# Optimization experiments

Hardware: AMD Instinct MI355X
Metric: run time of the kernel (lower is better)

Reference implementation:

```python
import jax, jax.numpy as jnp
import numpy as np

N_NODES = 49
FEAT_DIM = 1280            # efficientnet_v2_s feature dim
NODE_DIM = FEAT_DIM // N_NODES  # 26
GAT_HID = 256
HEADS = 4
NUM_CLASSES = 5
BATCH = 8192


def _grid_edges():
    # 7x7 grid, 8-neighborhood, as in _create_grid_edges, plus PyG default self loops
    edges = []
    for i in range(7):
        for j in range(7):
            node = i * 7 + j
            for di in (-1, 0, 1):
                for dj in (-1, 0, 1):
                    if di == 0 and dj == 0:
                        continue
                    ni, nj = i + di, j + dj
                    if 0 <= ni < 7 and 0 <= nj < 7:
                        edges.append((node, ni * 7 + nj))
    edges += [(n, n) for n in range(N_NODES)]  # add_self_loops=True (PyG default)
    return np.asarray(edges, dtype=np.int64).T  # [2, 361]


def setup_inputs() -> dict:
    key = jax.random.key(0)
    ks = jax.random.split(key, 16)
    s = 0.05
    inp = {
        "x": jax.random.normal(ks[0], (BATCH, FEAT_DIM), jnp.float32),
        "transform_w": jax.random.normal(ks[1], (FEAT_DIM, N_NODES * NODE_DIM), jnp.float32) * s,
        "transform_b": jnp.zeros((N_NODES * NODE_DIM,), jnp.float32),
        # GATv2 layer 1: 26 -> 64 per head, 4 heads, concat -> 256
        "g1_wl": jax.random.normal(ks[2], (NODE_DIM, GAT_HID), jnp.float32) * s,
        "g1_wr": jax.random.normal(ks[3], (NODE_DIM, GAT_HID), jnp.float32) * s,
        "g1_att": jax.random.normal(ks[4], (HEADS, GAT_HID // HEADS), jnp.float32) * s,
        "g1_b": jnp.zeros((GAT_HID,), jnp.float32),
        # GATv2 layer 2: 256 -> 256, 1 head, mean
        "g2_wl": jax.random.normal(ks[5], (GAT_HID, GAT_HID), jnp.float32) * s,
        "g2_wr": jax.random.normal(ks[6], (GAT_HID, GAT_HID), jnp.float32) * s,
        "g2_att": jax.random.normal(ks[7], (1, GAT_HID), jnp.float32) * s,
        "g2_b": jnp.zeros((GAT_HID,), jnp.float32),
        "fc_w": jax.random.normal(ks[8], (NODE_DIM + GAT_HID, NUM_CLASSES), jnp.float32) * s,
        "fc_b": jnp.zeros((NUM_CLASSES,), jnp.float32),
        "edge_index": jnp.asarray(_grid_edges()),
    }
    return inp


def _gatv2(x, src, dst, wl, wr, att, b, heads, out_ch, concat):
    # PyG GATv2Conv (share_weights=False, negative_slope=0.2, eval mode)
    n = x.shape[0]
    xl = (x @ wl).reshape(n, heads, out_ch)  # source messages
    xr = (x @ wr).reshape(n, heads, out_ch)  # target side of attention
    e = jax.nn.leaky_relu(xl[src] + xr[dst], 0.2)        # [E, H, C]
    score = jnp.einsum('ehc,hc->eh', e, att)             # [E, H]
    smax = jax.ops.segment_max(score, dst, num_segments=n)
    ex = jnp.exp(score - smax[dst])
    den = jax.ops.segment_sum(ex, dst, num_segments=n)
    alpha = ex / den[dst]                                # softmax over in-edges per node
    out = jax.ops.segment_sum(xl[src] * alpha[..., None], dst, num_segments=n)  # [N,H,C]
    out = out.reshape(n, heads * out_ch) if concat else out.mean(axis=1)
    return out + b


def reference(x, transform_w, transform_b, g1_wl, g1_wr, g1_att, g1_b,
              g2_wl, g2_wr, g2_att, g2_b, fc_w, fc_b, edge_index):
    src, dst = edge_index[0], edge_index[1]
    node = (x @ transform_w + transform_b).reshape(-1, N_NODES, NODE_DIM)  # [B,49,26]

    def graph(nf):
        h = _gatv2(nf, src, dst, g1_wl, g1_wr, g1_att, g1_b, HEADS, GAT_HID // HEADS, True)
        h = jax.nn.elu(h)  # dropout inactive in eval
        h = _gatv2(h, src, dst, g2_wl, g2_wr, g2_att, g2_b, 1, GAT_HID, False)
        return h  # [49, 256]

    g = jax.vmap(graph)(node)                              # [B,49,256]
    pooled = jnp.concatenate([node, g], axis=-1).mean(axis=1)  # [B, 282]
    return pooled @ fc_w + fc_b
```

## Files before the change

### kernel.cpp

```cpp
#include <hip/hip_runtime.h>
#include <hip/hip_bf16.h>

typedef __bf16 bf16;
typedef __attribute__((ext_vector_type(8))) __bf16 bf16x8;
typedef __attribute__((ext_vector_type(4))) float f32x4;

constexpr int BATCH = 8192, NN = 49, ND = 26, NOUT = 1274, FD = 1280;
constexpr int HID = 256, NE = 361, HEADS = 4;
constexpr int KT_X = 40;
constexpr int MT_X = 512;
constexpr int NB_W = 10;
constexpr int NTB  = 9;

constexpr size_t OFF_XPACK = 0;
constexpr size_t SZ_XPACK  = (size_t)MT_X * KT_X * 512 * 2;
constexpr size_t OFF_WPACK = OFF_XPACK + SZ_XPACK;
constexpr size_t SZ_WPACK  = (size_t)NB_W * NTB * KT_X * 512 * 2;
constexpr size_t OFF_B1    = OFF_WPACK + SZ_WPACK;
constexpr size_t SZ_B1     = (size_t)32 * 512 * 2;
constexpr size_t OFF_B2    = OFF_B1 + SZ_B1;
constexpr size_t SZ_B2     = (size_t)32 * 8 * 512 * 2;
constexpr size_t OFF_N32   = OFF_B2 + SZ_B2;
constexpr size_t SZ_N32    = (size_t)BATCH * NN * 32 * 2;
constexpr size_t OFF_PN    = OFF_N32 + SZ_N32;
constexpr size_t SZ_PN     = (size_t)BATCH * ND * 4;
constexpr size_t OFF_CSR   = OFF_PN + SZ_PN;
constexpr size_t SZ_CSR    = 8192;
constexpr size_t OFF_CHUNK = OFF_CSR + SZ_CSR;


__global__ __launch_bounds__(256) void k_pack_x(const float* __restrict__ x,
                                                bf16* __restrict__ xp) {
    int g = blockIdx.x * 256 + threadIdx.x;
    int lane = g & 63, frag = g >> 6;
    int mt = frag / KT_X, kt = frag - mt * KT_X;
    int row = mt * 16 + (lane & 15);
    int k0  = kt * 32 + (lane >> 4) * 8;
    const float* src = x + (size_t)row * FD + k0;
    bf16x8 v;
#pragma unroll
    for (int j = 0; j < 8; ++j) v[j] = (bf16)src[j];
    *(bf16x8*)(xp + ((size_t)frag * 64 + lane) * 8) = v;
}

__global__ __launch_bounds__(256) void k_pack_w(const float* __restrict__ w,
                                                bf16* __restrict__ wp) {
    int g = blockIdx.x * 256 + threadIdx.x;
    int lane = g & 63, frag = g >> 6;
    int kt = frag % KT_X, t2 = frag / KT_X;
    int nt = t2 % NTB, nb = t2 / NTB;
    int col = nb * 130 + nt * 16 + (lane & 15);
    int k0  = kt * 32 + (lane >> 4) * 8;
    bool ok = (col < NOUT) && (col < nb * 130 + 130);
    bf16x8 v;
#pragma unroll
    for (int j = 0; j < 8; ++j)
        v[j] = ok ? (bf16)w[(size_t)(k0 + j) * NOUT + col] : (bf16)0.f;
    *(bf16x8*)(wp + ((size_t)frag * 64 + lane) * 8) = v;
}

__global__ __launch_bounds__(256) void k_pack_g1(const float* __restrict__ wl,
                                                 const float* __restrict__ wr,
                                                 bf16* __restrict__ bp) {
    int g = blockIdx.x * 256 + threadIdx.x;
    int lane = g & 63, nt = g >> 6;
    int n  = nt * 16 + (lane & 15);
    int k0 = (lane >> 4) * 8;
    bf16x8 v;
#pragma unroll
    for (int j = 0; j < 8; ++j) {
        int k = k0 + j;
        float f = 0.f;
        if (k < ND) f = (n < HID) ? wl[k * HID + n] : wr[k * HID + (n - HID)];
        v[j] = (bf16)f;
    }
    *(bf16x8*)(bp + ((size_t)nt * 64 + lane) * 8) = v;
}

__global__ __launch_bounds__(256) void k_pack_g2(const float* __restrict__ wl,
                                                 const float* __restrict__ wr,
                                                 bf16* __restrict__ bp) {
    int g = blockIdx.x * 256 + threadIdx.x;
    int lane = g & 63, frag = g >> 6;
    int nt = frag >> 3, kt = frag & 7;
    int n  = nt * 16 + (lane & 15);
    int k0 = kt * 32 + (lane >> 4) * 8;
    bf16x8 v;
#pragma unroll
    for (int j = 0; j < 8; ++j) {
        int k = k0 + j;
        float f = (n < HID) ? wl[k * HID + n] : wr[k * HID + (n - HID)];
        v[j] = (bf16)f;
    }
    *(bf16x8*)(bp + ((size_t)frag * 64 + lane) * 8) = v;
}

__global__ __launch_bounds__(128) void k_csr_par(const int* __restrict__ ei,
                                                 int* __restrict__ csr) {
    __shared__ int es[NE], ed[NE], cnt[NN], ocnt[NN], off[NN + 1], ooff[NN + 1];
    int tid = threadIdx.x;
    if (tid < NN) { cnt[tid] = 0; ocnt[tid] = 0; }
    for (int e = tid; e < NE; e += 128) { es[e] = ei[e]; ed[e] = ei[NE + e]; }
    __syncthreads();
    for (int e = tid; e < NE; e += 128) {
        atomicAdd(&cnt[ed[e]], 1);
        atomicAdd(&ocnt[es[e]], 1);
    }
    __syncthreads();
    if (tid == 0) {
        off[0] = 0; ooff[0] = 0;
        for (int n = 0; n < NN; ++n) {
            off[n + 1] = off[n] + cnt[n];
            ooff[n + 1] = ooff[n] + ocnt[n];
        }
    }
    __syncthreads();
    if (tid < NN) {
        int p = off[tid];
        for (int e = 0; e < NE; ++e)
            if (ed[e] == tid) { csr[50 + p] = e; csr[411 + p] = es[e]; ++p; }
    } else if (tid >= 64 && tid < 64 + NN) {
        int n = tid - 64;
        int p = ooff[n];
        for (int e = 0; e < NE; ++e)
            if (es[e] == n) { csr[822 + p] = e; ++p; }
    }
    if (tid < 50) { csr[tid] = off[tid]; csr[772 + tid] = ooff[tid]; }
}

__global__ __launch_bounds__(256, 2) void k_gemm_node(const bf16* __restrict__ xp,
                                                      const bf16* __restrict__ wp,
                                                      const float* __restrict__ tb,
                                                      bf16* __restrict__ node32) {
    __shared__ bf16 L[128][148];
    __shared__ float tbS[144];
    int tid = threadIdx.x, lane = tid & 63, w = tid >> 6;
    int nb = blockIdx.y, C0 = nb * 130;
    int mt0 = blockIdx.x * 16 + w * 4;
    if (tid < 144) { int col = C0 + tid; tbS[tid] = (col < NOUT) ? tb[col] : 0.f; }
    f32x4 acc[4][9] = {};
    const bf16* wpB = wp + (size_t)(nb * NTB) * KT_X * 512;
    for (int kt = 0; kt < KT_X; ++kt) {
        bf16x8 a[4];
#pragma unroll
        for (int i = 0; i < 4; ++i)
            a[i] = *(const bf16x8*)(xp + (((size_t)(mt0 + i) * KT_X + kt) * 64 + lane) * 8);
#pragma unroll
        for (int j = 0; j < NTB; ++j) {
            bf16x8 b = *(const bf16x8*)(wpB + ((size_t)(j * KT_X + kt) * 64 + lane) * 8);
#pragma unroll
            for (int i = 0; i < 4; ++i)
                acc[i][j] = __builtin_amdgcn_mfma_f32_16x16x32_bf16(a[i], b, acc[i][j], 0, 0, 0);
        }
    }
    int c0 = lane & 15, r0 = (lane >> 4) * 4;
    int nodes = (nb == 9) ? 4 : 5;
    int total = 128 * nodes * 4;
    for (int half = 0; half < 2; ++half) {
        __syncthreads();
        if ((w >> 1) == half) {
            int lrbase = (w & 1) * 64;
#pragma unroll
            for (int i = 0; i < 4; ++i) {
#pragma unroll
                for (int j = 0; j < NTB; ++j) {
                    int col = j * 16 + c0;
                    float bias = tbS[col];
#pragma unroll
                    for (int r = 0; r < 4; ++r)
                        L[lrbase + i * 16 + r0 + r][col] = (bf16)(acc[i][j][r] + bias);
                }
            }
        }
        __syncthreads();
        int B0 = blockIdx.x * 256 + half * 128;
        for (int t = tid; t < total; t += 256) {
            int q = t & 3, t2 = t >> 2;
            int n_l = t2 % nodes, brow = t2 / nodes;
            bf16x8 o;
#pragma unroll
            for (int jj = 0; jj < 8; ++jj) {
                int d = q * 8 + jj;
                o[jj] = (d < ND) ? L[brow][n_l * 26 + d] : (bf16)0.f;
            }
            *(bf16x8*)(node32 + (((size_t)(B0 + brow) * NN + nb * 5 + n_l) * 32 + q * 8)) = o;
        }
    }
}

__global__ __launch_bounds__(256) void k_pool(const bf16* __restrict__ node32,
                                              float* __restrict__ pN) {
    int b = blockIdx.x * 8 + (threadIdx.x >> 5);
    int d = threadIdx.x & 31;
    if (d >= ND) return;
    const bf16* base = node32 + (size_t)b * NN * 32 + d;
    float s = 0.f;
    for (int n = 0; n < NN; ++n) s += (float)base[n * 32];
    pN[b * ND + d] = s;
}

__global__ __launch_bounds__(512, 2) void k_fuse1(const bf16* __restrict__ n32,
                                                  const bf16* __restrict__ B1p,
                                                  bf16* __restrict__ h1f,
                                                  const float* __restrict__ att1,
                                                  const float* __restrict__ g1b,
                                                  const int* __restrict__ ei,
                                                  const int* __restrict__ csr) {
    __shared__ __align__(16) char X[NN * 1024];
    __shared__ __align__(16) float attS[256];
    __shared__ float sc[NE * 4], srden[NN * 4], bS[256];
    __shared__ int ieOff[50], ieId[NE], ieSrc[NE], srcS[NE], dstS[NE];

    int tid = threadIdx.x, lane = tid & 63, w = tid >> 6, g = blockIdx.x;

    for (int i = tid; i < 256; i += 512) { attS[i] = att1[i]; bS[i] = g1b[i]; }
    for (int i = tid; i < NE; i += 512) {
        srcS[i] = ei[i]; dstS[i] = ei[NE + i];
        ieId[i] = csr[50 + i]; ieSrc[i] = csr[411 + i];
    }
    if (tid < 50) ieOff[tid] = csr[tid];

    {
        int mt = w & 3, ng = w >> 2;
        int arow = mt * 16 + (lane & 15);
        bf16x8 a = {};
        if (arow < NN)
            a = *(const bf16x8*)(n32 + ((size_t)(g * NN + arow) * 32 + (lane >> 4) * 8));
        f32x4 acc[16];
#pragma unroll
        for (int j = 0; j < 16; ++j) {
            f32x4 z = {0.f, 0.f, 0.f, 0.f};
            bf16x8 b = *(const bf16x8*)(B1p + ((size_t)(ng * 16 + j) * 64 + lane) * 8);
            acc[j] = __builtin_amdgcn_mfma_f32_16x16x32_bf16(a, b, z, 0, 0, 0);
        }
        int c0 = lane & 15, r0 = (lane >> 4) * 4;
#pragma unroll
        for (int j = 0; j < 16; ++j) {
            int col = (ng * 16 + j) * 16 + c0;
#pragma unroll
            for (int r = 0; r < 4; ++r) {
                int n = mt * 16 + r0 + r;
                if (n < NN)
                    *(bf16*)(X + n * 1024 + ((col * 2) ^ ((n & 7) << 4))) = (bf16)acc[j][r];
            }
        }
    }
    __syncthreads();

    int rot = tid & 7;
    for (int task = tid; task < NE * 4; task += 512) {
        int h = task / NE, e = task - h * NE;
        int s = srcS[e], d = dstS[e];
        int sws = (s & 7) << 4, swd = (d & 7) << 4;
        const char* ps = X + s * 1024;
        const char* pd = X + d * 1024;
        float pa[4] = {0.f, 0.f, 0.f, 0.f};
#pragma unroll
        for (int i = 0; i < 8; ++i) {
            int cc = ((i + rot) & 7) * 8;
            bf16x8 xl = *(const bf16x8*)(ps + (((h * 64 + cc) * 2) ^ sws));
            bf16x8 xr = *(const bf16x8*)(pd + (((256 + h * 64 + cc) * 2) ^ swd));
            float4 a0 = *(const float4*)(attS + h * 64 + cc);
            float4 a1 = *(const float4*)(attS + h * 64 + cc + 4);
            const float aa[8] = {a0.x, a0.y, a0.z, a0.w, a1.x, a1.y, a1.z, a1.w};
#pragma unroll
            for (int q = 0; q < 8; ++q) {
                float v = (float)xl[q] + (float)xr[q];
                v = v > 0.f ? v : 0.2f * v;
                pa[q & 3] = fmaf(aa[q], v, pa[q & 3]);
            }
        }
        sc[e * 4 + h] = (pa[0] + pa[1]) + (pa[2] + pa[3]);
    }
    __syncthreads();
    for (int t = tid; t < NN * 4; t += 512) {
        int n = t >> 2, h = t & 3;
        float m = -1e30f;
        for (int j = ieOff[n]; j < ieOff[n + 1]; ++j) m = fmaxf(m, sc[ieId[j] * 4 + h]);
        float den = 0.f;
        for (int j = ieOff[n]; j < ieOff[n + 1]; ++j) {
            int idx = ieId[j] * 4 + h;
            float ex = __expf(sc[idx] - m);
            sc[idx] = ex; den += ex;
        }
        srden[t] = 1.f / den;
    }
    __syncthreads();
    for (int task = tid; task < NN * 32; task += 512) {
        int n = task >> 5, cb = task & 31;
        int ch0 = cb * 8, hh = cb >> 3;
        float a8[8] = {};
        int j0 = ieOff[n], j1 = ieOff[n + 1];
        for (int j = j0; j < j1; ++j) {
            float al = sc[ieId[j] * 4 + hh];
            int s = ieSrc[j];
            bf16x8 xv = *(const bf16x8*)(X + s * 1024 + ((ch0 * 2) ^ ((s & 7) << 4)));
#pragma unroll
            for (int q = 0; q < 8; ++q) a8[q] = fmaf(al, (float)xv[q], a8[q]);
        }
        float rs = srden[n * 4 + hh];
        bf16x8 o;
#pragma unroll
        for (int q = 0; q < 8; ++q) {
            float v = fmaf(a8[q], rs, bS[ch0 + q]);
            v = v > 0.f ? v : (__expf(v) - 1.f);
            o[q] = (bf16)v;
        }
        int Rl = g * NN + n;
        int kt = ch0 >> 5, kg = (ch0 >> 3) & 3;
        size_t addr = (((size_t)(Rl >> 4) * 8 + kt) * 64 + (Rl & 15) + 16 * kg) * 8;
        *(bf16x8*)(h1f + addr) = o;
    }
}

__global__ __launch_bounds__(256) void k_gemm_l2(const bf16* __restrict__ Af,
                                                 const bf16* __restrict__ Bf,
                                                 bf16* __restrict__ xlr) {
    __shared__ bf16 LT[128][136];
    int tid = threadIdx.x, lane = tid & 63, w = tid >> 6;
    int mtb = blockIdx.x * 8 + (w >> 1) * 4;
    int ntb = blockIdx.y * 8 + (w & 1) * 4;
    f32x4 acc[4][4] = {};
    for (int kt = 0; kt < 8; ++kt) {
        bf16x8 a[4], b[4];
#pragma unroll
        for (int i = 0; i < 4; ++i)
            a[i] = *(const bf16x8*)(Af + (((size_t)(mtb + i) * 8 + kt) * 64 + lane) * 8);
#pragma unroll
        for (int j = 0; j < 4; ++j)
            b[j] = *(const bf16x8*)(Bf + (((size_t)(ntb + j) * 8 + kt) * 64 + lane) * 8);
#pragma unroll
        for (int i = 0; i < 4; ++i)
#pragma unroll
            for (int j = 0; j < 4; ++j)
                acc[i][j] = __builtin_amdgcn_mfma_f32_16x16x32_bf16(a[i], b[j], acc[i][j], 0, 0, 0);
    }
    int c0 = lane & 15, r0 = (lane >> 4) * 4;
    int lr0 = (w >> 1) * 64, lc0 = (w & 1) * 64;
#pragma unroll
    for (int i = 0; i < 4; ++i)
#pragma unroll
        for (int j = 0; j < 4; ++j)
#pragma unroll
            for (int r = 0; r < 4; ++r)
                LT[lr0 + i * 16 + r0 + r][lc0 + j * 16 + c0] = (bf16)acc[i][j][r];
    __syncthreads();
    size_t R0 = (size_t)blockIdx.x * 128, C0 = (size_t)blockIdx.y * 128;
#pragma unroll
    for (int it = 0; it < 8; ++it) {
        int idx = (it * 256 + tid) * 8;
        int r = idx >> 7, c = idx & 127;
        bf16x8 v = *(const bf16x8*)&LT[r][c];
        *(bf16x8*)(xlr + (R0 + r) * 512 + C0 + c) = v;
    }
}

__global__ __launch_bounds__(384) void k_score2(const bf16* __restrict__ xlr,
                                                const float* __restrict__ att2,
                                                const int* __restrict__ ei,
                                                float* __restrict__ scE) {
    __shared__ float attS[256];
    int tid = threadIdx.x, g = blockIdx.x;
    if (tid < 256) attS[tid] = att2[tid];
    __syncthreads();
    if (tid >= NE) return;
    int s = ei[tid], d = ei[NE + tid];
    const bf16* pl = xlr + ((size_t)g * NN + s) * 512;
    const bf16* pr = xlr + ((size_t)g * NN + d) * 512 + 256;
    float pa[4] = {0.f, 0.f, 0.f, 0.f};
#pragma unroll 4
    for (int i = 0; i < 32; ++i) {
        bf16x8 xl = *(const bf16x8*)(pl + i * 8);
        bf16x8 xr = *(const bf16x8*)(pr + i * 8);
#pragma unroll
        for (int q = 0; q < 8; ++q) {
            float v = (float)xl[q] + (float)xr[q];
            v = v > 0.f ? v : 0.2f * v;
            pa[q & 3] = fmaf(attS[i * 8 + q], v, pa[q & 3]);
        }
    }
    scE[(size_t)g * NE + tid] = (pa[0] + pa[1]) + (pa[2] + pa[3]);
}

__global__ __launch_bounds__(256) void k_soft2(const float* __restrict__ scE,
                                               const int* __restrict__ csr,
                                               float* __restrict__ sm,
                                               float* __restrict__ sr, int C) {
    int idx = blockIdx.x * 256 + threadIdx.x;
    int g = idx / NN, n = idx - g * NN;
    if (g >= C) return;
    const float* sg = scE + (size_t)g * NE;
    int j0 = csr[n], j1 = csr[n + 1];
    float m = -1e30f;
    for (int j = j0; j < j1; ++j) m = fmaxf(m, sg[csr[50 + j]]);
    float den = 0.f;
    for (int j = j0; j < j1; ++j) den += __expf(sg[csr[50 + j]] - m);
    sm[idx] = m; sr[idx] = 1.f / den;
}

__global__ __launch_bounds__(256) void k_wn(const float* __restrict__ scE,
                                            const int* __restrict__ csr,
                                            const int* __restrict__ ei,
                                            const float* __restrict__ sm,
                                            const float* __restrict__ sr,
                                            float* __restrict__ wN, int C) {
    int idx = blockIdx.x * 256 + threadIdx.x;
    int g = idx / NN, n = idx - g * NN;
    if (g >= C) return;
    const float* sg = scE + (size_t)g * NE;
    const float* smg = sm + (size_t)g * NN;
    const float* srg = sr + (size_t)g * NN;
    float wa = 0.f;
    int j0 = csr[772 + n], j1 = csr[772 + n + 1];
    for (int j = j0; j < j1; ++j) {
        int e = csr[822 + j];
        int d = ei[NE + e];
        wa += __expf(sg[e] - smg[d]) * srg[d];
    }
    wN[idx] = wa;
}

static __device__ __forceinline__ float waveReduceSum(float v) {
#pragma unroll
    for (int m = 32; m > 0; m >>= 1) v += __shfl_xor(v, m, 64);
    return v;
}

__global__ __launch_bounds__(256) void k_poolfc(const bf16* __restrict__ xlr,
                                                const float* __restrict__ wN,
                                                const float* __restrict__ pN,
                                                const float* __restrict__ g2b,
                                                const float* __restrict__ fcw,
                                                const float* __restrict__ fcb,
                                                int graph_base,
                                                float* __restrict__ out) {
    __shared__ float wSs[NN];
    __shared__ float poolS[288];
    int tid = threadIdx.x, g = blockIdx.x;
    if (tid < NN) wSs[tid] = wN[(size_t)g * NN + tid];
    if (tid >= 64 && tid < 64 + ND)
        poolS[tid - 64] = pN[(size_t)(graph_base + g) * ND + (tid - 64)] * (1.f / NN);
    __syncthreads();
    {
        const bf16* base = xlr + (size_t)g * NN * 512 + tid;
        float acc = 0.f;
        for (int n = 0; n < NN; ++n) acc = fmaf(wSs[n], (float)base[n * 512], acc);
        poolS[ND + tid] = acc * (1.f / NN) + g2b[tid];
    }
    __syncthreads();
    int w5 = tid >> 6, lane = tid & 63;
    for (int o = w5; o < 5; o += 4) {
        float a = 0.f;
        for (int d = lane; d < ND + HID; d += 64) a = fmaf(poolS[d], fcw[d * 5 + o], a);
        a = waveReduceSum(a);
        if (lane == 0) out[(size_t)(graph_base + g) * 5 + o] = a + fcb[o];
    }
}

extern "C" void kernel_launch(void* const* d_in, const int* in_sizes, int n_in,
                              void* d_out, int out_size, void* d_ws, size_t ws_size,
                              hipStream_t stream) {
    const float* x   = (const float*)d_in[0];
    const float* tw  = (const float*)d_in[1];
    const float* tb  = (const float*)d_in[2];
    const float* wl1 = (const float*)d_in[3];
    const float* wr1 = (const float*)d_in[4];
    const float* at1 = (const float*)d_in[5];
    const float* b1  = (const float*)d_in[6];
    const float* wl2 = (const float*)d_in[7];
    const float* wr2 = (const float*)d_in[8];
    const float* at2 = (const float*)d_in[9];
    const float* b2  = (const float*)d_in[10];
    const float* fcw = (const float*)d_in[11];
    const float* fcb = (const float*)d_in[12];
    const int*   ei  = (const int*)d_in[13];
    float* out = (float*)d_out;

    char* ws = (char*)d_ws;
    bf16*  xp   = (bf16*)(ws + OFF_XPACK);
    bf16*  wp   = (bf16*)(ws + OFF_WPACK);
    bf16*  b1p  = (bf16*)(ws + OFF_B1);
    bf16*  b2p  = (bf16*)(ws + OFF_B2);
    bf16*  n32  = (bf16*)(ws + OFF_N32);
    float* pN   = (float*)(ws + OFF_PN);
    int*   csr  = (int*)(ws + OFF_CSR);

    const size_t perC = 50176 + 12544 + 1444 + 3 * 196;
    int C = 512;
    for (int cand : {2048, 1024, 512}) {
        if (OFF_CHUNK + (size_t)cand * perC <= ws_size) { C = cand; break; }
    }
    bf16*  xlr = (bf16*)(ws + OFF_CHUNK);
    bf16*  h1f = (bf16*)(ws + OFF_CHUNK + (size_t)C * 50176);
    float* scE = (float*)(ws + OFF_CHUNK + (size_t)C * (50176 + 12544));
    float* smB = scE + (size_t)C * NE;
    float* srB = smB + (size_t)C * NN;
    float* wNB = srB + (size_t)C * NN;
    int nchunks = BATCH / C;
    int MtC = C * NN / 16;
    int gnBlocks = (C * NN + 255) / 256;

    k_pack_x<<<dim3(MT_X * KT_X * 64 / 256), dim3(256), 0, stream>>>(x, xp);
    k_pack_w<<<dim3(NB_W * NTB * KT_X * 64 / 256), dim3(256), 0, stream>>>(tw, wp);
    k_pack_g1<<<dim3(8), dim3(256), 0, stream>>>(wl1, wr1, b1p);
    k_pack_g2<<<dim3(64), dim3(256), 0, stream>>>(wl2, wr2, b2p);
    k_csr_par<<<dim3(1), dim3(128), 0, stream>>>(ei, csr);
    k_gemm_node<<<dim3(32, NB_W), dim3(256), 0, stream>>>(xp, wp, tb, n32);
    k_pool<<<dim3(BATCH / 8), dim3(256), 0, stream>>>(n32, pN);

    for (int c = 0; c < nchunks; ++c) {
        const bf16* n32c = n32 + (size_t)c * C * NN * 32;
        k_fuse1<<<dim3(C), dim3(512), 0, stream>>>(n32c, b1p, h1f, at1, b1, ei, csr);
        k_gemm_l2<<<dim3(MtC / 8, 4), dim3(256), 0, stream>>>(h1f, b2p, xlr);
        k_score2<<<dim3(C), dim3(384), 0, stream>>>(xlr, at2, ei, scE);
        k_soft2<<<dim3(gnBlocks), dim3(256), 0, stream>>>(scE, csr, smB, srB, C);
        k_wn<<<dim3(gnBlocks), dim3(256), 0, stream>>>(scE, csr, ei, smB, srB, wNB, C);
        k_poolfc<<<dim3(C), dim3(256), 0, stream>>>(xlr, wNB, pN, b2, fcw, fcb,
                                                    c * C, out);
    }
}
```

Baseline: 1.034 ms.

## Stage layer-2 features in LDS, fuse softmax and weight kernels, vectorize layer-1 stores

k_score2 now copies each graph's 49x512 bf16 features into swizzled shared memory before computing edge scores, so the scattered global reads repeated per edge become LDS reads. The softmax-statistics and per-node weight kernels are merged into one block-per-graph kernel that keeps max and reciprocal denominator in shared memory, which drops a launch and the global round trip for those arrays. In k_fuse1 the MFMA operands are swapped so each lane holds four consecutive channels of one row and writes them as one 8-byte store instead of four scalar stores. In exchange, k_score2 uses about 49KB of LDS per block, which can lower occupancy, and the new 64-thread softwn blocks leave 15 of 64 lanes idle.

```diff
diff --git a/kernel.cpp b/kernel.cpp
--- a/kernel.cpp
+++ b/kernel.cpp
@@ -3,6 +3,7 @@
 
 typedef __bf16 bf16;
 typedef __attribute__((ext_vector_type(8))) __bf16 bf16x8;
+typedef __attribute__((ext_vector_type(4))) __bf16 bf16x4;
 typedef __attribute__((ext_vector_type(4))) float f32x4;
 
 constexpr int BATCH = 8192, NN = 49, ND = 26, NOUT = 1274, FD = 1280;
@@ -222,26 +223,24 @@
 
     {
         int mt = w & 3, ng = w >> 2;
-        int arow = mt * 16 + (lane & 15);
-        bf16x8 a = {};
-        if (arow < NN)
-            a = *(const bf16x8*)(n32 + ((size_t)(g * NN + arow) * 32 + (lane >> 4) * 8));
-        f32x4 acc[16];
+        int m = mt * 16 + (lane & 15);
+        bf16x8 bfrag = {};
+        if (m < NN)
+            bfrag = *(const bf16x8*)(n32 + ((size_t)(g * NN + m) * 32 + (lane >> 4) * 8));
+        int chq = (lane >> 4) * 4;
+        int sw = (m & 7) << 4;
+        char* rowp = X + m * 1024;
 #pragma unroll
         for (int j = 0; j < 16; ++j) {
             f32x4 z = {0.f, 0.f, 0.f, 0.f};
-            bf16x8 b = *(const bf16x8*)(B1p + ((size_t)(ng * 16 + j) * 64 + lane) * 8);
-            acc[j] = __builtin_amdgcn_mfma_f32_16x16x32_bf16(a, b, z, 0, 0, 0);
-        }
-        int c0 = lane & 15, r0 = (lane >> 4) * 4;
-#pragma unroll
-        for (int j = 0; j < 16; ++j) {
-            int col = (ng * 16 + j) * 16 + c0;
-#pragma unroll
-            for (int r = 0; r < 4; ++r) {
-                int n = mt * 16 + r0 + r;
-                if (n < NN)
-                    *(bf16*)(X + n * 1024 + ((col * 2) ^ ((n & 7) << 4))) = (bf16)acc[j][r];
+            bf16x8 afrag = *(const bf16x8*)(B1p + ((size_t)(ng * 16 + j) * 64 + lane) * 8);
+            f32x4 acc = __builtin_amdgcn_mfma_f32_16x16x32_bf16(afrag, bfrag, z, 0, 0, 0);
+            if (m < NN) {
+                int ch = (ng * 16 + j) * 16 + chq;
+                bf16x4 o4;
+#pragma unroll
+                for (int r = 0; r < 4; ++r) o4[r] = (bf16)acc[r];
+                *(bf16x4*)(rowp + ((ch * 2) ^ sw)) = o4;
             }
         }
     }
@@ -359,65 +358,67 @@
                                                 const float* __restrict__ att2,
                                                 const int* __restrict__ ei,
                                                 float* __restrict__ scE) {
+    __shared__ __align__(16) char X[NN * 1024];
     __shared__ float attS[256];
     int tid = threadIdx.x, g = blockIdx.x;
+    const char* srcp = (const char*)(xlr + (size_t)g * NN * 512);
+    for (int off = tid * 16; off < NN * 1024; off += 384 * 16) {
+        int row = off >> 10;
+        *(uint4*)(X + (off ^ ((row & 7) << 4))) = *(const uint4*)(srcp + off);
+    }
     if (tid < 256) attS[tid] = att2[tid];
     __syncthreads();
     if (tid >= NE) return;
     int s = ei[tid], d = ei[NE + tid];
-    const bf16* pl = xlr + ((size_t)g * NN + s) * 512;
-    const bf16* pr = xlr + ((size_t)g * NN + d) * 512 + 256;
+    int sws = (s & 7) << 4, swd = (d & 7) << 4;
+    const char* ps = X + s * 1024;
+    const char* pd = X + d * 1024;
+    int rot = tid & 7;
     float pa[4] = {0.f, 0.f, 0.f, 0.f};
-#pragma unroll 4
+#pragma unroll 8
     for (int i = 0; i < 32; ++i) {
-        bf16x8 xl = *(const bf16x8*)(pl + i * 8);
-        bf16x8 xr = *(const bf16x8*)(pr + i * 8);
+        int cc = ((i + rot) & 31) * 8;
+        bf16x8 xl = *(const bf16x8*)(ps + ((cc * 2) ^ sws));
+        bf16x8 xr = *(const bf16x8*)(pd + (((256 + cc) * 2) ^ swd));
+        float4 a0 = *(const float4*)(attS + cc);
+        float4 a1 = *(const float4*)(attS + cc + 4);
+        const float aa[8] = {a0.x, a0.y, a0.z, a0.w, a1.x, a1.y, a1.z, a1.w};
 #pragma unroll
         for (int q = 0; q < 8; ++q) {
             float v = (float)xl[q] + (float)xr[q];
             v = v > 0.f ? v : 0.2f * v;
-            pa[q & 3] = fmaf(attS[i * 8 + q], v, pa[q & 3]);
+            pa[q & 3] = fmaf(aa[q], v, pa[q & 3]);
         }
     }
     scE[(size_t)g * NE + tid] = (pa[0] + pa[1]) + (pa[2] + pa[3]);
 }
 
-__global__ __launch_bounds__(256) void k_soft2(const float* __restrict__ scE,
+__global__ __launch_bounds__(64) void k_softwn(const float* __restrict__ scE,
                                                const int* __restrict__ csr,
-                                               float* __restrict__ sm,
-                                               float* __restrict__ sr, int C) {
-    int idx = blockIdx.x * 256 + threadIdx.x;
-    int g = idx / NN, n = idx - g * NN;
-    if (g >= C) return;
+                                               const int* __restrict__ ei,
+                                               float* __restrict__ wN) {
+    __shared__ float sm[NN], sr[NN];
+    int g = blockIdx.x, tid = threadIdx.x;
     const float* sg = scE + (size_t)g * NE;
-    int j0 = csr[n], j1 = csr[n + 1];
-    float m = -1e30f;
-    for (int j = j0; j < j1; ++j) m = fmaxf(m, sg[csr[50 + j]]);
-    float den = 0.f;
-    for (int j = j0; j < j1; ++j) den += __expf(sg[csr[50 + j]] - m);
-    sm[idx] = m; sr[idx] = 1.f / den;
-}
-
-__global__ __launch_bounds__(256) void k_wn(const float* __restrict__ scE,
-                                            const int* __restrict__ csr,
-                                            const int* __restrict__ ei,
-                                            const float* __restrict__ sm,
-                                            const float* __restrict__ sr,
-                                            float* __restrict__ wN, int C) {
-    int idx = blockIdx.x * 256 + threadIdx.x;
-    int g = idx / NN, n = idx - g * NN;
-    if (g >= C) return;
-    const float* sg = scE + (size_t)g * NE;
-    const float* smg = sm + (size_t)g * NN;
-    const float* srg = sr + (size_t)g * NN;
-    float wa = 0.f;
-    int j0 = csr[772 + n], j1 = csr[772 + n + 1];
-    for (int j = j0; j < j1; ++j) {
-        int e = csr[822 + j];
-        int d = ei[NE + e];
-        wa += __expf(sg[e] - smg[d]) * srg[d];
-    }
-    wN[idx] = wa;
+    if (tid < NN) {
+        int j0 = csr[tid], j1 = csr[tid + 1];
+        float m = -1e30f;
+        for (int j = j0; j < j1; ++j) m = fmaxf(m, sg[csr[50 + j]]);
+        float den = 0.f;
+        for (int j = j0; j < j1; ++j) den += __expf(sg[csr[50 + j]] - m);
+        sm[tid] = m; sr[tid] = 1.f / den;
+    }
+    __syncthreads();
+    if (tid < NN) {
+        float wa = 0.f;
+        int j0 = csr[772 + tid], j1 = csr[772 + tid + 1];
+        for (int j = j0; j < j1; ++j) {
+            int e = csr[822 + j];
+            int d = ei[NE + e];
+            wa += __expf(sg[e] - sm[d]) * sr[d];
+        }
+        wN[(size_t)g * NN + tid] = wa;
+    }
 }
 
 static __device__ __forceinline__ float waveReduceSum(float v) {
@@ -485,7 +486,7 @@
     float* pN   = (float*)(ws + OFF_PN);
     int*   csr  = (int*)(ws + OFF_CSR);
 
-    const size_t perC = 50176 + 12544 + 1444 + 3 * 196;
+    const size_t perC = 50176 + 12544 + 1444 + 196;
     int C = 512;
     for (int cand : {2048, 1024, 512}) {
         if (OFF_CHUNK + (size_t)cand * perC <= ws_size) { C = cand; break; }
@@ -493,12 +494,9 @@
     bf16*  xlr = (bf16*)(ws + OFF_CHUNK);
     bf16*  h1f = (bf16*)(ws + OFF_CHUNK + (size_t)C * 50176);
     float* scE = (float*)(ws + OFF_CHUNK + (size_t)C * (50176 + 12544));
-    float* smB = scE + (size_t)C * NE;
-    float* srB = smB + (size_t)C * NN;
-    float* wNB = srB + (size_t)C * NN;
+    float* wNB = scE + (size_t)C * NE;
     int nchunks = BATCH / C;
     int MtC = C * NN / 16;
-    int gnBlocks = (C * NN + 255) / 256;
 
     k_pack_x<<<dim3(MT_X * KT_X * 64 / 256), dim3(256), 0, stream>>>(x, xp);
     k_pack_w<<<dim3(NB_W * NTB * KT_X * 64 / 256), dim3(256), 0, stream>>>(tw, wp);
@@ -513,8 +511,7 @@
         k_fuse1<<<dim3(C), dim3(512), 0, stream>>>(n32c, b1p, h1f, at1, b1, ei, csr);
         k_gemm_l2<<<dim3(MtC / 8, 4), dim3(256), 0, stream>>>(h1f, b2p, xlr);
         k_score2<<<dim3(C), dim3(384), 0, stream>>>(xlr, at2, ei, scE);
-        k_soft2<<<dim3(gnBlocks), dim3(256), 0, stream>>>(scE, csr, smB, srB, C);
-        k_wn<<<dim3(gnBlocks), dim3(256), 0, stream>>>(scE, csr, ei, smB, srB, wNB, C);
+        k_softwn<<<dim3(C), dim3(64), 0, stream>>>(scE, csr, ei, wNB);
         k_poolfc<<<dim3(C), dim3(256), 0, stream>>>(xlr, wNB, pN, b2, fcw, fcb,
                                                     c * C, out);
     }
```

Result: faster. 944.0 us (-8.7%).
